# Kernel tuning notes

Measured on AMD Instinct MI355X. Metric: run time of the kernel, lower is better.

Reference implementation:

```python
import jax, jax.numpy as jnp
import numpy as np
from jax import lax

MAX_OBJ = 100
IOU_THRES = 0.45
SCORE_THRES = 0.25
MAX_WH = 7680.0

# xywh -> xyxy conversion matrix (same as ONNX_ORT.convert_matrix)
CONVERT = jnp.array([[1, 0, 1, 0],
                     [0, 1, 0, 1],
                     [-0.5, 0, 0.5, 0],
                     [0, -0.5, 0, 0.5]], dtype=jnp.float32)


def _iou_one_vs_all(box, boxes):
    # box: [4] xyxy, boxes: [N,4] xyxy
    x1 = jnp.maximum(box[0], boxes[:, 0])
    y1 = jnp.maximum(box[1], boxes[:, 1])
    x2 = jnp.minimum(box[2], boxes[:, 2])
    y2 = jnp.minimum(box[3], boxes[:, 3])
    inter = jnp.clip(x2 - x1, 0.0) * jnp.clip(y2 - y1, 0.0)
    a = (box[2] - box[0]) * (box[3] - box[1])
    b = (boxes[:, 2] - boxes[:, 0]) * (boxes[:, 3] - boxes[:, 1])
    return inter / (a + b - inter + 1e-9)


def _nms_indices(nmsbox, max_score):
    # Greedy class-offset NMS; returns [MAX_OBJ] indices, -1 for padding.
    valid0 = max_score >= SCORE_THRES

    def step(valid, _):
        s = jnp.where(valid, max_score, -1.0)
        i = jnp.argmax(s)
        ok = s[i] >= SCORE_THRES
        iou = _iou_one_vs_all(nmsbox[i], nmsbox)
        valid = valid & (iou <= IOU_THRES)
        valid = valid.at[i].set(False)
        return valid, jnp.where(ok, i, -1)

    _, idxs = lax.scan(step, valid0, None, length=MAX_OBJ)
    return idxs


def _forward(x1, x2, num_labels1, num_labels2):
    B, N1, _ = x1.shape
    N2 = x2.shape[1]
    # pad x1 class scores with zeros for model2's labels (appended at end)
    x1p = jnp.concatenate([x1, jnp.zeros((B, N1, num_labels2), x1.dtype)], axis=2)
    # pad x2: insert zeros for model1's labels between conf and its own classes
    x2p = jnp.concatenate([x2[:, :, 0:5],
                           jnp.zeros((B, N2, num_labels1), x2.dtype),
                           x2[:, :, 5:]], axis=2)
    x = jnp.concatenate([x1p, x2p], axis=1)  # [B, N1+N2, 5+C1+C2]

    boxes = x[:, :, :4] @ CONVERT            # xywh -> xyxy, [B,N,4]
    conf = x[:, :, 4:5]
    scores = x[:, :, 5:] * conf              # [B,N,C]
    max_score = scores.max(axis=2)           # [B,N]
    cat_id = scores.argmax(axis=2)           # [B,N]
    # class-offset boxes so NMS is class-aware
    nmsbox = boxes + cat_id[..., None].astype(boxes.dtype) * MAX_WH

    idxs = jax.vmap(_nms_indices)(lax.stop_gradient(nmsbox),
                                  lax.stop_gradient(max_score))  # [B,MAX_OBJ]
    mask = idxs >= 0
    si = jnp.maximum(idxs, 0)
    sel_boxes = jnp.take_along_axis(boxes, si[..., None], axis=1)      # [B,MAX_OBJ,4]
    sel_cat = jnp.take_along_axis(cat_id, si, axis=1).astype(boxes.dtype)
    sel_score = jnp.take_along_axis(max_score, si, axis=1)

    mf = mask.astype(boxes.dtype)
    Xcol = jnp.where(mask, jnp.arange(B)[:, None], -1).astype(boxes.dtype)
    out = jnp.concatenate([Xcol[..., None],
                           sel_boxes * mf[..., None],
                           (sel_cat * mf)[..., None],
                           (sel_score * mf)[..., None]], axis=2)
    return out.reshape(B * MAX_OBJ, 7)


def setup_inputs() -> dict:
    key = jax.random.key(0)
    k1, k2 = jax.random.split(key)
    x1 = jax.random.uniform(k1, (4, 25200, 85), dtype=jnp.float32)
    x2 = jax.random.uniform(k2, (4, 25200, 25), dtype=jnp.float32)
    return {"x1": x1, "x2": x2, "num_labels1": 80, "num_labels2": 20}


def reference(x1, x2, num_labels1, num_labels2):
    return _forward(x1, x2, num_labels1, num_labels2)
```

## Files before the change

### kernel.cpp

```cpp
#include <hip/hip_runtime.h>
#include <stdint.h>

#pragma clang fp contract(off)

#define BATCH 4
#define N1 25200
#define NROW 50400
#define NCLS 100
#define TOT (BATCH*NROW)
#define CAPB 1280
#define SCORE_T 0.25f
#define IOU_T 0.45f
#define MAXWH 7680.0f

#define X1_SLAB 64
#define X1_SPB 394
#define X2_SLAB 256
#define X2_SPB 99

#define BIN_SLICES 128
#define BIN_SL 394

typedef unsigned long long u64;

__device__ __forceinline__ u64 pack_key(unsigned sb, int n, int cid) {
    return ((u64)sb << 32) | ((u64)(unsigned)((n ^ 0xFFFF) & 0xFFFF) << 8) | (u64)(unsigned)cid;
}

__device__ __forceinline__ bool sup_test(float inter, float sum) {
    float d = (sum - inter) + 1e-9f;
    float t1 = IOU_T * d;
    bool hi = inter > t1 * 1.00001f;
    bool lo = inter < t1 * 0.99999f;
    if (__builtin_expect(!(hi || lo), 0)) return (inter / d) > IOU_T;
    return hi;
}

__device__ __forceinline__ float rl(float v, int srcLane) {
    return __int_as_float(__builtin_amdgcn_readlane(__float_as_int(v), srcLane));
}

__device__ __forceinline__ void blk2bucket(int blk, int& b, int& c) {
    if (blk < BATCH * 20) { b = blk / 20; c = 80 + (blk - b * 20); }
    else { int z = blk - BATCH * 20; b = z / 80; c = z - b * 80; }
}

__device__ __forceinline__ int prefix_ge(const u64* list, int cnt, u64 T) {
    int lo = 0, hi = cnt;
    while (lo < hi) {
        int mid = (lo + hi) >> 1;
        if (list[mid] >= T) lo = mid + 1; else hi = mid;
    }
    return lo;
}

__device__ __forceinline__ void sort_desc(u64* sk, int L, int t) {
    bool act = (t * 8) < L;
    u64 r[8];
    if (act) {
#pragma unroll
        for (int e = 0; e < 8; ++e) r[e] = sk[t * 8 + e];
    }
    for (int k = 2; k <= L; k <<= 1) {
        for (int j = k >> 1; j > 0; j >>= 1) {
            if (j >= 512) {
                if (act) {
#pragma unroll
                    for (int e = 0; e < 8; ++e) sk[t * 8 + e] = r[e];
                }
                __syncthreads();
                if (act) {
                    bool iAmLo = (t & (j >> 3)) == 0;
                    bool descSeg = (t & (k >> 3)) == 0;
                    bool takeMax = (descSeg == iAmLo);
#pragma unroll
                    for (int e = 0; e < 8; ++e) {
                        u64 u = r[e];
                        u64 v = sk[(t * 8 + e) ^ j];
                        bool uGE = (u >= v);
                        r[e] = (takeMax == uGE) ? u : v;
                    }
                }
                __syncthreads();
            } else if (j >= 8) {
                if (act) {
                    int dt = j >> 3;
                    bool iAmLo = (t & dt) == 0;
                    bool descSeg = (t & (k >> 3)) == 0;
                    bool takeMax = (descSeg == iAmLo);
#pragma unroll
                    for (int e = 0; e < 8; ++e) {
                        u64 u = r[e];
                        u64 v = __shfl_xor(u, dt, 64);
                        bool uGE = (u >= v);
                        r[e] = (takeMax == uGE) ? u : v;
                    }
                }
            } else {
                if (act) {
#pragma unroll
                    for (int e = 0; e < 8; ++e) {
                        if (!(e & j)) {
                            int e2 = e | j;
                            bool descSeg = (k >= 8) ? ((t & (k >> 3)) == 0)
                                                    : ((e & k) == 0);
                            u64 lo = r[e], hi = r[e2];
                            bool sw = descSeg ? (lo < hi) : (lo > hi);
                            if (sw) { r[e] = hi; r[e2] = lo; }
                        }
                    }
                }
            }
        }
    }
    if (act) {
#pragma unroll
        for (int e = 0; e < 8; ++e) sk[t * 8 + e] = r[e];
    }
    __syncthreads();
}

__global__ __launch_bounds__(256) void k_rows(const float* __restrict__ x1,
                                              const float* __restrict__ x2,
                                              float4* __restrict__ boxes4,
                                              u64* __restrict__ rowKey) {
    __shared__ float4 ld4[1600];
    float* ld = (float*)ld4;
    int blk = blockIdx.x;
    int t = threadIdx.x;
    const int NX1 = BATCH * X1_SPB;
    if (blk < NX1) {
        int b = blk / X1_SPB, s = blk - b * X1_SPB;
        int r0 = s * X1_SLAB;
        int nr = min(X1_SLAB, N1 - r0);
        const float4* src = (const float4*)(x1 + ((size_t)b * N1 + r0) * 85);
        int count4 = (nr * 85) >> 2;
        if (count4 == 1360) {
            float4 v0 = src[t], v1 = src[t + 256], v2 = src[t + 512];
            float4 v3 = src[t + 768], v4 = src[t + 1024];
            float4 v5;
            bool h5 = (t < 80);
            if (h5) v5 = src[t + 1280];
            ld4[t] = v0; ld4[t + 256] = v1; ld4[t + 512] = v2;
            ld4[t + 768] = v3; ld4[t + 1024] = v4;
            if (h5) ld4[t + 1280] = v5;
        } else {
            for (int i = t; i < count4; i += 256) ld4[i] = src[i];
        }
        __syncthreads();
        int row = t >> 2, sub = t & 3;
        if (row < nr) {
            const float* p = ld + row * 85;
            float conf = p[4];
            u64 key = 0ULL;
            int base = sub * 20;
            for (int c = 0; c < 20; ++c) {
                int j = base + c;
                float v = p[5 + j] * conf;
                u64 kk = ((u64)__float_as_uint(v) << 32) | (unsigned)~(unsigned)j;
                if (kk > key) key = kk;
            }
            u64 o;
            o = __shfl_xor(key, 1, 64); if (o > key) key = o;
            o = __shfl_xor(key, 2, 64); if (o > key) key = o;
            if (sub == 0) {
                float best = __uint_as_float((unsigned)(key >> 32));
                int bestj = ~(unsigned)key;
                int n = r0 + row;
                int r = b * NROW + n;
                u64 outk = 0ULL;
                if (best >= SCORE_T) {
                    float cx = p[0], cy = p[1], w = p[2], h = p[3];
                    boxes4[r] = make_float4(cx - 0.5f * w, cy - 0.5f * h,
                                            cx + 0.5f * w, cy + 0.5f * h);
                    outk = pack_key((unsigned)(key >> 32), n, bestj);
                }
                rowKey[r] = outk;
            }
        }
    } else {
        int blk2 = blk - NX1;
        int b = blk2 / X2_SPB, s = blk2 - b * X2_SPB;
        int r0 = s * X2_SLAB;
        int nr = min(X2_SLAB, N1 - r0);
        const float4* src = (const float4*)(x2 + ((size_t)b * N1 + r0) * 25);
        int count4 = (nr * 25) >> 2;
        if (count4 == 1600) {
            float4 v0 = src[t], v1 = src[t + 256], v2 = src[t + 512];
            float4 v3 = src[t + 768], v4 = src[t + 1024], v5 = src[t + 1280];
            float4 v6;
            bool h6 = (t < 64);
            if (h6) v6 = src[t + 1536];
            ld4[t] = v0; ld4[t + 256] = v1; ld4[t + 512] = v2;
            ld4[t + 768] = v3; ld4[t + 1024] = v4; ld4[t + 1280] = v5;
            if (h6) ld4[t + 1536] = v6;
        } else {
            for (int i = t; i < count4; i += 256) ld4[i] = src[i];
        }
        __syncthreads();
        if (t < nr) {
            const float* p = ld + t * 25;
            float conf = p[4];
            float best = 0.0f; int bestj = 0;
            for (int j2 = 0; j2 < 20; ++j2) {
                float v = p[5 + j2] * conf;
                if (v > best) { best = v; bestj = 80 + j2; }
            }
            int n = N1 + r0 + t;
            int r = b * NROW + n;
            u64 outk = 0ULL;
            if (best >= SCORE_T) {
                float cx = p[0], cy = p[1], w = p[2], h = p[3];
                boxes4[r] = make_float4(cx - 0.5f * w, cy - 0.5f * h,
                                        cx + 0.5f * w, cy + 0.5f * h);
                outk = pack_key(__float_as_uint(best), n, bestj);
            }
            rowKey[r] = outk;
        }
    }
}

__global__ __launch_bounds__(256) void k_bin(const u64* __restrict__ rowKey,
                                             u64* __restrict__ csrKey,
                                             int* __restrict__ fill) {
    __shared__ u64 keys[BIN_SL];
    __shared__ int cnt[NCLS];
    __shared__ int base[NCLS];
    __shared__ int cur[NCLS];
    int blk = blockIdx.x;
    int b = blk / BIN_SLICES, s = blk - b * BIN_SLICES;
    int r0 = s * BIN_SL;
    int nr = min(BIN_SL, NROW - r0);
    int t = threadIdx.x;
    if (t < NCLS) { cnt[t] = 0; cur[t] = 0; }
    __syncthreads();
    const u64* src = rowKey + (size_t)b * NROW + r0;
    for (int i = t; i < nr; i += 256) {
        u64 k = src[i];
        keys[i] = k;
        if (k != 0ULL) atomicAdd(&cnt[(int)(k & 0xFF)], 1);
    }
    __syncthreads();
    if (t < NCLS && cnt[t] > 0)
        base[t] = atomicAdd(&fill[b * NCLS + t], cnt[t]);
    __syncthreads();
    for (int i = t; i < nr; i += 256) {
        u64 k = keys[i];
        if (k != 0ULL) {
            int c = (int)(k & 0xFF);
            int p = base[c] + atomicAdd(&cur[c], 1);
            if (p < CAPB) csrKey[(size_t)(b * NCLS + c) * CAPB + p] = k;
        }
    }
}

__global__ __launch_bounds__(256) void k_sort(u64* __restrict__ csrKey,
                                              const int* __restrict__ fill,
                                              int* __restrict__ accCnt) {
    __shared__ u64 sk[2048];
    int b, c; blk2bucket(blockIdx.x, b, c);
    int bucket = b * NCLS + c;
    int t = threadIdx.x;
    int cnt0 = min(fill[bucket], CAPB);
    if (cnt0 == 0) { if (t == 0) accCnt[bucket] = 0; return; }
    u64* src = csrKey + (size_t)bucket * CAPB;
    int L = 512; while (L < cnt0) L <<= 1;
    for (int i = t; i < L; i += 256) sk[i] = (i < cnt0) ? src[i] : 0ULL;
    __syncthreads();
    sort_desc(sk, L, t);
    for (int i = t; i < cnt0; i += 256) src[i] = sk[i];
}

__global__ __launch_bounds__(64) void k_greedy(const float4* __restrict__ boxes4,
                                               const u64* __restrict__ csrKey,
                                               const int* __restrict__ fill,
                                               u64* __restrict__ accKey,
                                               int* __restrict__ accCnt) {
    __shared__ float4 accQ[100];
    __shared__ float accA[100];
    int b, c; blk2bucket(blockIdx.x, b, c);
    int bucket = b * NCLS + c;
    int lane = threadIdx.x;
    int cnt0 = min(fill[bucket], CAPB);
    if (cnt0 == 0) { if (lane == 0) accCnt[bucket] = 0; return; }
    const u64* skB = csrKey + (size_t)bucket * CAPB;
    float off = (float)c * MAXWH;
    u64 curKey = (lane < cnt0) ? skB[lane] : 0ULL;
    float4 curBox = make_float4(0.f, 0.f, 0.f, 0.f);
    if (lane < cnt0) {
        int n = 0xFFFF ^ (int)((curKey >> 8) & 0xFFFF);
        curBox = boxes4[b * NROW + n];
    }
    int m = 0;
    for (int base = 0; base < cnt0 && m < 100; base += 64) {
        int j = base + lane;
        bool alive = (j < cnt0);
        u64 myKey = curKey;
        float4 a = curBox;
        a.x += off; a.y += off; a.z += off; a.w += off;
        float aA = (a.z - a.x) * (a.w - a.y);
        int jn = j + 64;
        u64 nk = (jn < cnt0) ? skB[jn] : 0ULL;
        int k2 = 0;
        while (k2 < m) {
            if (__ballot(alive) == 0ULL) break;
            int rem = m - k2;
            if (rem >= 8) {
#pragma unroll
                for (int u = 0; u < 8; ++u) {
                    float4 q = accQ[k2 + u];
                    float qa = accA[k2 + u];
                    float xx1 = fmaxf(a.x, q.x), yy1 = fmaxf(a.y, q.y);
                    float xx2 = fminf(a.z, q.z), yy2 = fminf(a.w, q.w);
                    float inter = fmaxf(xx2 - xx1, 0.f) * fmaxf(yy2 - yy1, 0.f);
                    alive = alive && !sup_test(inter, qa + aA);
                }
                k2 += 8;
            } else {
                for (int u = 0; u < rem; ++u) {
                    float4 q = accQ[k2 + u];
                    float qa = accA[k2 + u];
                    float xx1 = fmaxf(a.x, q.x), yy1 = fmaxf(a.y, q.y);
                    float xx2 = fminf(a.z, q.z), yy2 = fminf(a.w, q.w);
                    float inter = fmaxf(xx2 - xx1, 0.f) * fmaxf(yy2 - yy1, 0.f);
                    alive = alive && !sup_test(inter, qa + aA);
                }
                k2 = m;
            }
        }
        float4 nb = make_float4(0.f, 0.f, 0.f, 0.f);
        if (jn < cnt0) {
            int nn = 0xFFFF ^ (int)((nk >> 8) & 0xFFFF);
            nb = boxes4[b * NROW + nn];
        }
        u64 av = __ballot(alive);
        int accIdx = -1;
        while (av != 0ULL && m < 100) {
            int f = __builtin_ctzll(av);
            float qx = rl(a.x, f), qy = rl(a.y, f);
            float qz = rl(a.z, f), qw = rl(a.w, f);
            if (lane == f) { accIdx = m; alive = false; }
            ++m;
            if (alive) {
                float qa = (qz - qx) * (qw - qy);
                float xx1 = fmaxf(a.x, qx), yy1 = fmaxf(a.y, qy);
                float xx2 = fminf(a.z, qz), yy2 = fminf(a.w, qw);
                float inter = fmaxf(xx2 - xx1, 0.f) * fmaxf(yy2 - yy1, 0.f);
                alive = !sup_test(inter, qa + aA);
            }
            av = __ballot(alive);
        }
        if (accIdx >= 0) {
            accQ[accIdx] = a; accA[accIdx] = aA;
            accKey[(size_t)bucket * 100 + accIdx] = myKey;
        }
        curKey = nk; curBox = nb;
    }
    if (lane == 0) accCnt[bucket] = m;
}

__global__ __launch_bounds__(256) void k_merge(const float4* __restrict__ boxes4,
                                               const u64* __restrict__ accKey,
                                               const int* __restrict__ accCnt,
                                               float* __restrict__ out) {
    __shared__ u64 sk[1024];
    __shared__ u64 head[NCLS];
    __shared__ int cnts[NCLS];
    __shared__ int pc[NCLS];
    int b = blockIdx.x, t = threadIdx.x;
    const u64* base = accKey + (size_t)b * NCLS * 100;
    if (t < NCLS) {
        int cc = accCnt[b * NCLS + t];
        cnts[t] = cc;
        head[t] = (cc > 0) ? base[t * 100] : 0ULL;
    }
    __syncthreads();
    int S = 0, ne = 0; u64 mn = ~0ULL;
    for (int c = 0; c < NCLS; ++c) {
        int cc = cnts[c];
        S += cc;
        if (cc > 0) { ++ne; u64 h = head[c]; if (h < mn) mn = h; }
    }
    u64 T;
    bool bisect;
    if (S <= 900)            { T = 0ULL; bisect = false; }
    else if (ne == NCLS)     { T = mn;   bisect = false; }
    else                     { T = 0ULL; bisect = true;  }
    if (t < NCLS) pc[t] = bisect ? 0 : prefix_ge(base + t * 100, cnts[t], T);
    __syncthreads();
    int G = 0;
    for (int c = 0; c < NCLS; ++c) G += pc[c];
    if (G > 1000) bisect = true;
    if (bisect) {
        u64 lo = 0ULL, hi = ~0ULL;
        for (int it = 0; it < 64; ++it) {
            u64 mid = lo + ((hi - lo) >> 1);
            if (t < NCLS) pc[t] = prefix_ge(base + t * 100, cnts[t], mid);
            __syncthreads();
            int cnt = 0;
            for (int c = 0; c < NCLS; ++c) cnt += pc[c];
            if (cnt >= 100 && cnt <= 1000) { T = mid; G = cnt; break; }
            if (cnt < 100) hi = mid; else lo = mid;
            __syncthreads();
        }
    }
    if (t < NCLS) {
        int off = 0;
        for (int c = 0; c < t; ++c) off += pc[c];
        int p = pc[t];
        for (int j = 0; j < p; ++j) sk[off + j] = base[t * 100 + j];
    }
    for (int i = G + t; i < 1024; i += 256) sk[i] = 0ULL;
    __syncthreads();
    sort_desc(sk, 1024, t);
    if (t < 100) {
        u64 k = sk[t];
        float* o7 = out + (size_t)(b * 100 + t) * 7;
        if (k == 0ULL) {
            o7[0] = -1.0f;
            o7[1] = 0.0f; o7[2] = 0.0f; o7[3] = 0.0f;
            o7[4] = 0.0f; o7[5] = 0.0f; o7[6] = 0.0f;
        } else {
            int n = 0xFFFF ^ (int)((k >> 8) & 0xFFFF);
            int cid = (int)(k & 0xFF);
            float4 bx = boxes4[b * NROW + n];
            o7[0] = (float)b;
            o7[1] = bx.x; o7[2] = bx.y; o7[3] = bx.z; o7[4] = bx.w;
            o7[5] = (float)cid;
            o7[6] = __uint_as_float((unsigned)(k >> 32));
        }
    }
}

extern "C" void kernel_launch(void* const* d_in, const int* in_sizes, int n_in,
                              void* d_out, int out_size, void* d_ws, size_t ws_size,
                              hipStream_t stream) {
    const float* x1 = (const float*)d_in[0];
    const float* x2 = (const float*)d_in[1];
    float* out = (float*)d_out;

    float4* boxes4 = (float4*)d_ws;
    u64* rowKey = (u64*)(boxes4 + TOT);
    u64* csrKey = rowKey + TOT;
    u64* accKey = csrKey + (size_t)BATCH * NCLS * CAPB;
    int* fill   = (int*)(accKey + (size_t)BATCH * NCLS * 100);
    int* accCnt = fill + BATCH * NCLS;

    hipMemsetAsync(fill, 0, sizeof(int) * BATCH * NCLS, stream);

    int rowBlocks = BATCH * X1_SPB + BATCH * X2_SPB;
    k_rows<<<rowBlocks, 256, 0, stream>>>(x1, x2, boxes4, rowKey);
    k_bin<<<BATCH * BIN_SLICES, 256, 0, stream>>>(rowKey, csrKey, fill);
    k_sort<<<BATCH * NCLS, 256, 0, stream>>>(csrKey, fill, accCnt);
    k_greedy<<<BATCH * NCLS, 64, 0, stream>>>(boxes4, csrKey, fill, accKey, accCnt);
    k_merge<<<BATCH, 256, 0, stream>>>(boxes4, accKey, accCnt, out);
}
```

Measured before the change: 136.7 us.

## Replace serial in-wavefront greedy NMS with suppression bitmask rows and scalar resolve

The intra-chunk greedy NMS loop is restructured. It used to pick each survivor serially and recompute IoU against the remaining lanes after every pick. Now each lane first builds a 64-bit suppression row against every surviving candidate ranked below it. The greedy acceptance is then resolved with scalar readlane and mask operations, and each accepted lane computes its slot with a popcount. This removes the per-acceptance ballot and vector IoU dependency chain, at the cost of always computing up to 64 IoUs per chunk even when few candidates survive.

Result: slower. 143.4 us (+4.9%).

```diff
diff --git a/kernel.cpp b/kernel.cpp
--- a/kernel.cpp
+++ b/kernel.cpp
@@ -334,26 +334,40 @@
             nb = boxes4[b * NROW + nn];
         }
         u64 av = __ballot(alive);
-        int accIdx = -1;
-        while (av != 0ULL && m < 100) {
-            int f = __builtin_ctzll(av);
-            float qx = rl(a.x, f), qy = rl(a.y, f);
-            float qz = rl(a.z, f), qw = rl(a.w, f);
-            if (lane == f) { accIdx = m; alive = false; }
-            ++m;
-            if (alive) {
-                float qa = (qz - qx) * (qw - qy);
-                float xx1 = fmaxf(a.x, qx), yy1 = fmaxf(a.y, qy);
-                float xx2 = fminf(a.z, qz), yy2 = fminf(a.w, qw);
-                float inter = fmaxf(xx2 - xx1, 0.f) * fmaxf(yy2 - yy1, 0.f);
-                alive = !sup_test(inter, qa + aA);
-            }
-            av = __ballot(alive);
-        }
-        if (accIdx >= 0) {
+        u64 myRow = 0ULL;
+        u64 tmp = av;
+        while (tmp) {
+            int sj = __builtin_ctzll(tmp); tmp &= tmp - 1ULL;
+            float qx = rl(a.x, sj), qy = rl(a.y, sj);
+            float qz = rl(a.z, sj), qw = rl(a.w, sj);
+            float qa = rl(aA, sj);
+            float xx1 = fmaxf(a.x, qx), yy1 = fmaxf(a.y, qy);
+            float xx2 = fminf(a.z, qz), yy2 = fminf(a.w, qw);
+            float inter = fmaxf(xx2 - xx1, 0.f) * fmaxf(yy2 - yy1, 0.f);
+            bool sup = (sj > lane) && sup_test(inter, qa + aA);
+            myRow |= ((u64)sup) << sj;
+        }
+        u64 rem = av;
+        u64 acceptedMask = 0ULL;
+        int mNew = m;
+        while (rem != 0ULL && mNew < 100) {
+            int f = __builtin_ctzll(rem);
+            acceptedMask |= 1ULL << f;
+            ++mNew;
+            unsigned rlo = (unsigned)__builtin_amdgcn_readlane(
+                (int)(unsigned)(myRow & 0xFFFFFFFFULL), f);
+            unsigned rhi = (unsigned)__builtin_amdgcn_readlane(
+                (int)(unsigned)(myRow >> 32), f);
+            u64 rowf = ((u64)rhi << 32) | (u64)rlo;
+            rem &= ~rowf;
+            rem &= ~(1ULL << f);
+        }
+        if (alive && ((acceptedMask >> lane) & 1ULL)) {
+            int accIdx = m + __popcll(acceptedMask & ((1ULL << lane) - 1ULL));
             accQ[accIdx] = a; accA[accIdx] = aA;
             accKey[(size_t)bucket * 100 + accIdx] = myKey;
         }
+        m = mNew;
         curKey = nk; curBox = nb;
     }
     if (lane == 0) accCnt[bucket] = m;
```
